# Optimization experiments

Measured on AMD Instinct MI355X. Metric: run time of the kernel, lower is better.

The kernel has to match this reference:

```python
import jax, jax.numpy as jnp
import numpy as np

L = 4            # l1 = l2 = lambd = 4
M = 2 * L + 1    # 9 m-channels
N = 4096         # environment pairs
D = 256          # feature channels
K = 100          # number of nonzero real-CG terms


def setup_inputs() -> dict:
    key = jax.random.key(0)
    k1, k2, k3, k4, k5, k6 = jax.random.split(key, 6)
    X1 = jax.random.normal(k1, (M, N, D), dtype=jnp.float32)
    X2 = jax.random.normal(k2, (M, N, D), dtype=jnp.float32)
    m1_aligned = jax.random.randint(k3, (K,), 0, M)
    m2_aligned = jax.random.randint(k4, (K,), 0, M)
    mu = jnp.sort(jax.random.randint(k5, (K,), 0, M))  # appended in mu order in the torch init
    multipliers = jax.random.normal(k6, (K,), dtype=jnp.float32)
    return {"X1": X1, "X2": X2, "m1_aligned": m1_aligned,
            "m2_aligned": m2_aligned, "mu": mu, "multipliers": multipliers}


def reference(X1, X2, m1_aligned, m2_aligned, mu, multipliers):
    # gather along m-dim, elementwise multiply by CG multipliers  -> [K, N, D]
    contributions = X1[m1_aligned] * X2[m2_aligned] * multipliers[:, None, None]
    # scatter-add into the 2*lambd+1 output channels (mu is sorted)
    result = jax.ops.segment_sum(contributions, mu, num_segments=M,
                                 indices_are_sorted=True)
    return result  # [2*lambd+1, N, D]
```

## Files before the change

### kernel.cpp

```cpp
#include <hip/hip_runtime.h>


#define M_CH 9
#define TILE 256
#define THREADS 64
#define TPB 4
#define PLAN_PAD 128

typedef const void __attribute__((address_space(1))) * gcptr;
typedef void       __attribute__((address_space(3))) * lsptr;

__global__ __launch_bounds__(128) void prep_kernel(
    const int* __restrict__ m1, const int* __restrict__ m2,
    const int* __restrict__ mu, const float* __restrict__ mult,
    int K, int* __restrict__ ws) {
    __shared__ int smu[PLAN_PAD];
    int t = threadIdx.x;
    if (t < K) smu[t] = mu[t];
    __syncthreads();
    int4* plan = (int4*)(ws + 16);
    if (t < K) {
        int4 e;
        e.x = m1[t] * (TILE * 4);
        e.y = (M_CH + m2[t]) * (TILE * 4);
        e.z = __float_as_int(mult[t]);
        e.w = 0;
        plan[t] = e;
    } else if (t < PLAN_PAD) {
        int4 e; e.x = 0; e.y = M_CH * TILE * 4; e.z = 0; e.w = 0;
        plan[t] = e;
    }
    if (t <= M_CH) {
        int c = 0;
        for (int k = 0; k < K; ++k) c += (smu[k] < t) ? 1 : 0;
        ws[t] = c;
    }
}

__device__ __forceinline__ void stage_tile(float* dst, const float* s1,
                                           const float* s2, int P, int tid) {
    #pragma unroll
    for (int m = 0; m < M_CH; ++m) {
        __builtin_amdgcn_global_load_lds((gcptr)(s1 + m * P),
                                         (lsptr)(dst + m * TILE + tid * 4), 16, 0, 0);
        __builtin_amdgcn_global_load_lds((gcptr)(s2 + m * P),
                                         (lsptr)(dst + (M_CH + m) * TILE + tid * 4), 16, 0, 0);
    }
}

__global__ __launch_bounds__(THREADS) void cleb_kernel(
    const float* __restrict__ X1, const float* __restrict__ X2,
    const int* __restrict__ ws, float* __restrict__ out, int P) {
    __shared__ float lds[2][2 * M_CH * TILE];
    const int tid = threadIdx.x;
    const int base0 = blockIdx.x * (TILE * TPB);

    stage_tile(lds[0], X1 + base0 + tid * 4, X2 + base0 + tid * 4, P, tid);

    int seg[M_CH + 1];
    #pragma unroll
    for (int i = 0; i <= M_CH; ++i) seg[i] = ws[i];
    const int4* plan = (const int4*)(ws + 16);
    const int lane_off = tid * 16;

    #pragma unroll
    for (int t = 0; t < TPB; ++t) {
        const int base = base0 + t * TILE;
        if (t + 1 < TPB) {
            stage_tile(lds[(t + 1) & 1], X1 + base + TILE + tid * 4,
                       X2 + base + TILE + tid * 4, P, tid);
            asm volatile("s_waitcnt vmcnt(18)" ::: "memory");
        } else {
            asm volatile("s_waitcnt vmcnt(0)" ::: "memory");
        }
        __builtin_amdgcn_sched_barrier(0);

        const char* ldsb = (const char*)lds[t & 1];
        float* outp = out + base + tid * 4;

        #pragma unroll
        for (int m = 0; m < M_CH; ++m) {
            float4 acc = make_float4(0.f, 0.f, 0.f, 0.f);
            const int s_ = seg[m], e_ = seg[m + 1];
            int4 pe = plan[s_];
            #pragma unroll 4
            for (int k = s_; k < e_; ++k) {
                int4 pn = plan[k + 1];
                const float4 a = *(const float4*)(ldsb + pe.x + lane_off);
                const float4 b = *(const float4*)(ldsb + pe.y + lane_off);
                const float c = __int_as_float(pe.z);
                acc.x = fmaf(c * a.x, b.x, acc.x);
                acc.y = fmaf(c * a.y, b.y, acc.y);
                acc.z = fmaf(c * a.z, b.z, acc.z);
                acc.w = fmaf(c * a.w, b.w, acc.w);
                pe = pn;
            }
            *(float4*)(outp + m * P) = acc;
        }
    }
}

extern "C" void kernel_launch(void* const* d_in, const int* in_sizes, int n_in,
                              void* d_out, int out_size, void* d_ws, size_t ws_size,
                              hipStream_t stream) {
    const float* X1   = (const float*)d_in[0];
    const float* X2   = (const float*)d_in[1];
    const int*   m1   = (const int*)d_in[2];
    const int*   m2   = (const int*)d_in[3];
    const int*   mu   = (const int*)d_in[4];
    const float* mult = (const float*)d_in[5];
    float* out = (float*)d_out;
    int*   ws  = (int*)d_ws;

    const int K = in_sizes[2];
    const int P = in_sizes[0] / M_CH;

    prep_kernel<<<1, 128, 0, stream>>>(m1, m2, mu, mult, K, ws);
    cleb_kernel<<<P / (TILE * TPB), THREADS, 0, stream>>>(X1, X2, ws, out, P);
}
```

Measured before the change: 135.4 us.

## Pad CG plan per channel to multiples of four and single-buffer LDS tiles

```diff
diff --git a/kernel.cpp b/kernel.cpp
--- a/kernel.cpp
+++ b/kernel.cpp
@@ -4,8 +4,9 @@
 #define M_CH 9
 #define TILE 256
 #define THREADS 64
-#define TPB 4
+#define TPB 2
 #define PLAN_PAD 128
+#define ROWB (TILE * 4)
 
 typedef const void __attribute__((address_space(1))) * gcptr;
 typedef void       __attribute__((address_space(3))) * lsptr;
@@ -15,85 +16,114 @@
     const int* __restrict__ mu, const float* __restrict__ mult,
     int K, int* __restrict__ ws) {
     __shared__ int smu[PLAN_PAD];
-    int t = threadIdx.x;
+    __shared__ int s_len[16], s_pstart[16];
+    const int t = threadIdx.x;
     if (t < K) smu[t] = mu[t];
     __syncthreads();
+    if (t < M_CH) {
+        int c = 0;
+        for (int k = 0; k < K; ++k) c += (smu[k] == t) ? 1 : 0;
+        s_len[t] = c;
+    }
+    __syncthreads();
+    if (t == 0) {
+        int acc = 0;
+        for (int m = 0; m < M_CH; ++m) {
+            s_pstart[m] = acc;
+            acc += (s_len[m] + 3) & ~3;
+        }
+        s_pstart[M_CH] = acc;
+    }
+    __syncthreads();
+    if (t <= M_CH) ws[t] = s_pstart[t];
     int4* plan = (int4*)(ws + 16);
+    if (t < PLAN_PAD) {
+        int4 e; e.x = 0; e.y = M_CH * ROWB; e.z = 0; e.w = 0;
+        plan[t] = e;
+    }
+    __syncthreads();
     if (t < K) {
+        int r = 0;
+        for (int k = 0; k < t; ++k) r += (smu[k] == smu[t]) ? 1 : 0;
         int4 e;
-        e.x = m1[t] * (TILE * 4);
-        e.y = (M_CH + m2[t]) * (TILE * 4);
+        e.x = m1[t] * ROWB;
+        e.y = (M_CH + m2[t]) * ROWB;
         e.z = __float_as_int(mult[t]);
         e.w = 0;
-        plan[t] = e;
-    } else if (t < PLAN_PAD) {
-        int4 e; e.x = 0; e.y = M_CH * TILE * 4; e.z = 0; e.w = 0;
-        plan[t] = e;
-    }
-    if (t <= M_CH) {
-        int c = 0;
-        for (int k = 0; k < K; ++k) c += (smu[k] < t) ? 1 : 0;
-        ws[t] = c;
-    }
-}
-
-__device__ __forceinline__ void stage_tile(float* dst, const float* s1,
-                                           const float* s2, int P, int tid) {
-    #pragma unroll
-    for (int m = 0; m < M_CH; ++m) {
-        __builtin_amdgcn_global_load_lds((gcptr)(s1 + m * P),
-                                         (lsptr)(dst + m * TILE + tid * 4), 16, 0, 0);
-        __builtin_amdgcn_global_load_lds((gcptr)(s2 + m * P),
-                                         (lsptr)(dst + (M_CH + m) * TILE + tid * 4), 16, 0, 0);
+        plan[s_pstart[smu[t]] + r] = e;
     }
 }
 
 __global__ __launch_bounds__(THREADS) void cleb_kernel(
     const float* __restrict__ X1, const float* __restrict__ X2,
     const int* __restrict__ ws, float* __restrict__ out, int P) {
-    __shared__ float lds[2][2 * M_CH * TILE];
+    __shared__ float lds[2 * M_CH * TILE];
     const int tid = threadIdx.x;
     const int base0 = blockIdx.x * (TILE * TPB);
-
-    stage_tile(lds[0], X1 + base0 + tid * 4, X2 + base0 + tid * 4, P, tid);
 
     int seg[M_CH + 1];
     #pragma unroll
     for (int i = 0; i <= M_CH; ++i) seg[i] = ws[i];
     const int4* plan = (const int4*)(ws + 16);
+    const char* ldsb = (const char*)lds;
     const int lane_off = tid * 16;
 
     #pragma unroll
     for (int t = 0; t < TPB; ++t) {
         const int base = base0 + t * TILE;
-        if (t + 1 < TPB) {
-            stage_tile(lds[(t + 1) & 1], X1 + base + TILE + tid * 4,
-                       X2 + base + TILE + tid * 4, P, tid);
-            asm volatile("s_waitcnt vmcnt(18)" ::: "memory");
-        } else {
-            asm volatile("s_waitcnt vmcnt(0)" ::: "memory");
+        const float* s1 = X1 + base + tid * 4;
+        const float* s2 = X2 + base + tid * 4;
+        asm volatile("s_waitcnt lgkmcnt(0)" ::: "memory");
+        __builtin_amdgcn_sched_barrier(0);
+        #pragma unroll
+        for (int m = 0; m < M_CH; ++m) {
+            __builtin_amdgcn_global_load_lds((gcptr)(s1 + m * P),
+                                             (lsptr)(lds + m * TILE + tid * 4), 16, 0, 0);
+            __builtin_amdgcn_global_load_lds((gcptr)(s2 + m * P),
+                                             (lsptr)(lds + (M_CH + m) * TILE + tid * 4), 16, 0, 0);
         }
+        asm volatile("s_waitcnt vmcnt(0)" ::: "memory");
         __builtin_amdgcn_sched_barrier(0);
 
-        const char* ldsb = (const char*)lds[t & 1];
         float* outp = out + base + tid * 4;
-
         #pragma unroll
         for (int m = 0; m < M_CH; ++m) {
             float4 acc = make_float4(0.f, 0.f, 0.f, 0.f);
             const int s_ = seg[m], e_ = seg[m + 1];
-            int4 pe = plan[s_];
-            #pragma unroll 4
-            for (int k = s_; k < e_; ++k) {
-                int4 pn = plan[k + 1];
-                const float4 a = *(const float4*)(ldsb + pe.x + lane_off);
-                const float4 b = *(const float4*)(ldsb + pe.y + lane_off);
-                const float c = __int_as_float(pe.z);
-                acc.x = fmaf(c * a.x, b.x, acc.x);
-                acc.y = fmaf(c * a.y, b.y, acc.y);
-                acc.z = fmaf(c * a.z, b.z, acc.z);
-                acc.w = fmaf(c * a.w, b.w, acc.w);
-                pe = pn;
+            #pragma unroll 2
+            for (int k = s_; k < e_; k += 4) {
+                const int4 e0 = plan[k + 0];
+                const int4 e1 = plan[k + 1];
+                const int4 e2 = plan[k + 2];
+                const int4 e3 = plan[k + 3];
+                const float4 a0 = *(const float4*)(ldsb + e0.x + lane_off);
+                const float4 b0 = *(const float4*)(ldsb + e0.y + lane_off);
+                const float4 a1 = *(const float4*)(ldsb + e1.x + lane_off);
+                const float4 b1 = *(const float4*)(ldsb + e1.y + lane_off);
+                const float4 a2 = *(const float4*)(ldsb + e2.x + lane_off);
+                const float4 b2 = *(const float4*)(ldsb + e2.y + lane_off);
+                const float4 a3 = *(const float4*)(ldsb + e3.x + lane_off);
+                const float4 b3 = *(const float4*)(ldsb + e3.y + lane_off);
+                const float c0 = __int_as_float(e0.z);
+                const float c1 = __int_as_float(e1.z);
+                const float c2 = __int_as_float(e2.z);
+                const float c3 = __int_as_float(e3.z);
+                acc.x = fmaf(c0 * a0.x, b0.x, acc.x);
+                acc.y = fmaf(c0 * a0.y, b0.y, acc.y);
+                acc.z = fmaf(c0 * a0.z, b0.z, acc.z);
+                acc.w = fmaf(c0 * a0.w, b0.w, acc.w);
+                acc.x = fmaf(c1 * a1.x, b1.x, acc.x);
+                acc.y = fmaf(c1 * a1.y, b1.y, acc.y);
+                acc.z = fmaf(c1 * a1.z, b1.z, acc.z);
+                acc.w = fmaf(c1 * a1.w, b1.w, acc.w);
+                acc.x = fmaf(c2 * a2.x, b2.x, acc.x);
+                acc.y = fmaf(c2 * a2.y, b2.y, acc.y);
+                acc.z = fmaf(c2 * a2.z, b2.z, acc.z);
+                acc.w = fmaf(c2 * a2.w, b2.w, acc.w);
+                acc.x = fmaf(c3 * a3.x, b3.x, acc.x);
+                acc.y = fmaf(c3 * a3.y, b3.y, acc.y);
+                acc.z = fmaf(c3 * a3.z, b3.z, acc.z);
+                acc.w = fmaf(c3 * a3.w, b3.w, acc.w);
             }
             *(float4*)(outp + m * P) = acc;
         }
```

Result: no change. 135.7 us (+0.2%).
